# Kernel tuning notes

Measured on AMD Instinct MI355X. Metric: run time of the kernel, lower is better.

Reference implementation:

```python
import jax, jax.numpy as jnp
import numpy as np

N_NODES = 100000
N_EDGES = 1000000
D = 64
OUT = 64
EPS = 1e-5


def setup_inputs() -> dict:
    key = jax.random.key(0)
    k1, k2, k3, k4 = jax.random.split(key, 4)
    x = jax.random.normal(k1, (N_NODES, D), dtype=jnp.float32)
    edge_index = jax.random.randint(k2, (2, N_EDGES), 0, N_NODES, dtype=jnp.int64)
    # Linear(2*D, OUT): torch default init ~ U(-1/sqrt(fan_in), 1/sqrt(fan_in))
    bound = 1.0 / np.sqrt(2 * D)
    W = jax.random.uniform(k3, (2 * D, OUT), minval=-bound, maxval=bound, dtype=jnp.float32)
    b = jax.random.uniform(k4, (OUT,), minval=-bound, maxval=bound, dtype=jnp.float32)
    gamma = jnp.ones((OUT,), dtype=jnp.float32)
    beta = jnp.zeros((OUT,), dtype=jnp.float32)
    return {"x": x, "edge_index": edge_index, "W": W, "b": b, "gamma": gamma, "beta": beta}


def reference(x, edge_index, W, b, gamma, beta):
    row, col = edge_index[0], edge_index[1]
    # gather source features and scatter-add into destination nodes
    neighbor_sum = jax.ops.segment_sum(x[row], col, num_segments=x.shape[0])  # [N, D]
    h = jnp.concatenate([x, neighbor_sum], axis=-1)  # [N, 2D]
    h = h @ W + b  # [N, OUT]
    # LayerNorm over last dim
    mu = jnp.mean(h, axis=-1, keepdims=True)
    var = jnp.var(h, axis=-1, keepdims=True)
    h = (h - mu) * jax.lax.rsqrt(var + EPS) * gamma + beta
    return h
```

## Files before the change

kernel.cpp:

```cpp
#include <hip/hip_runtime.h>

#define NN 100000
#define NE 1000000
#define OUT_D 64
#define EPS 1e-5f

#define NB 196
#define COLS 512
#define BSTRIDE 6016
#define PBSTRIDE 8064
#define EPB 4096
#define NBLK1 245
#define NPROJ 1024

typedef __attribute__((ext_vector_type(8))) short bf16x8;
typedef __attribute__((ext_vector_type(4))) float f32x4;
typedef __attribute__((ext_vector_type(4))) int i32x4;

static __device__ __forceinline__ unsigned short f2bf(float f) {
    unsigned u = __float_as_uint(f);
    u += 0x7FFFu + ((u >> 16) & 1u);
    return (unsigned short)(u >> 16);
}
static __device__ __forceinline__ float bf2f(unsigned short s) {
    return __uint_as_float((unsigned)s << 16);
}

__global__ __launch_bounds__(256) void mega_kernel(
    const float* __restrict__ x, const float* __restrict__ W,
    const int* __restrict__ ei, int* __restrict__ gcur, unsigned* __restrict__ gbuf,
    unsigned short* __restrict__ y1, unsigned short* __restrict__ y2)
{
    const int tid = threadIdx.x;
    const int lane = tid & 63;
    const int wv = tid >> 6;

    if (blockIdx.x < NBLK1) {
        __shared__ int lcnt[NB];
        __shared__ int loff[NB + 1];
        __shared__ int lbase[NB];
        __shared__ int lcur[NB];
        __shared__ int wpart[4];
        __shared__ unsigned lbuf[EPB];
        __shared__ unsigned char lbkt[EPB];
        const int e0 = blockIdx.x * EPB;

        int rows[16], cols[16];
        #pragma unroll
        for (int j = 0; j < 16; ++j) {
            const int e = e0 + j * 256 + tid;
            const bool v = e < NE;
            rows[j] = v ? ei[e] : 0;
            cols[j] = v ? ei[NE + e] : -1;
        }
        for (int i = tid; i < NB; i += 256) lcnt[i] = 0;
        __syncthreads();
        #pragma unroll
        for (int j = 0; j < 16; ++j)
            if (cols[j] >= 0) atomicAdd(&lcnt[cols[j] >> 9], 1);
        __syncthreads();
        {
            const int c = (tid < NB) ? lcnt[tid] : 0;
            int s = c;
            #pragma unroll
            for (int o = 1; o < 64; o <<= 1) { int t = __shfl_up(s, o); if (lane >= o) s += t; }
            if (lane == 63) wpart[wv] = s;
            __syncthreads();
            int woff = 0;
            for (int ww = 0; ww < wv; ++ww) woff += wpart[ww];
            if (tid < NB) {
                loff[tid] = woff + s - c;
                lcur[tid] = woff + s - c;
                lbase[tid] = atomicAdd(&gcur[tid], c);
            }
            if (tid == NB - 1) loff[NB] = woff + s;
        }
        __syncthreads();
        #pragma unroll
        for (int j = 0; j < 16; ++j) {
            if (cols[j] >= 0) {
                const int b = cols[j] >> 9;
                const int p = atomicAdd(&lcur[b], 1);
                lbuf[p] = ((unsigned)rows[j] << 9) | (unsigned)(cols[j] & (COLS - 1));
                lbkt[p] = (unsigned char)b;
            }
        }
        __syncthreads();
        const int total = loff[NB];
        for (int t = tid; t < total; t += 256) {
            const int b = lbkt[t];
            const unsigned idx = (unsigned)(lbase[b] + (t - loff[b]));
            if (idx < BSTRIDE) gbuf[(size_t)b * BSTRIDE + idx] = lbuf[t];
        }
    } else {
        const int m = lane & 15;
        const int quad = lane >> 4;
        bf16x8 Wf[8][2];
        #pragma unroll
        for (int t = 0; t < 8; ++t)
            #pragma unroll
            for (int q = 0; q < 2; ++q) {
                bf16x8 f;
                #pragma unroll
                for (int j = 0; j < 8; ++j) {
                    const int k = q * 32 + quad * 8 + j;
                    const int krow = (t < 4) ? k : (64 + k);
                    const int col = (t & 3) * 16 + m;
                    f[j] = (short)f2bf(W[krow * 64 + col]);
                }
                Wf[t][q] = f;
            }
        for (int tile = (blockIdx.x - NBLK1) * 4 + wv; tile < NN / 16; tile += NPROJ * 4) {
            const int n0 = tile * 16;
            bf16x8 Af[2];
            #pragma unroll
            for (int q = 0; q < 2; ++q) {
                const float* px = x + (size_t)(n0 + m) * 64 + q * 32 + quad * 8;
                const f32x4 a0 = *(const f32x4*)px;
                const f32x4 a1 = *(const f32x4*)(px + 4);
                bf16x8 f;
                #pragma unroll
                for (int j = 0; j < 4; ++j) { f[j] = (short)f2bf(a0[j]); f[4 + j] = (short)f2bf(a1[j]); }
                Af[q] = f;
            }
            #pragma unroll
            for (int t = 0; t < 8; ++t) {
                f32x4 acc = {0.f, 0.f, 0.f, 0.f};
                acc = __builtin_amdgcn_mfma_f32_16x16x32_bf16(Af[0], Wf[t][0], acc, 0, 0, 0);
                acc = __builtin_amdgcn_mfma_f32_16x16x32_bf16(Af[1], Wf[t][1], acc, 0, 0, 0);
                unsigned short* __restrict__ dst = (t < 4) ? y1 : y2;
                const int colb = (t & 3) * 16 + m;
                #pragma unroll
                for (int r = 0; r < 4; ++r)
                    dst[(size_t)(n0 + quad * 4 + r) * 64 + colb] = f2bf(acc[r]);
            }
        }
    }
}

__global__ __launch_bounds__(256) void place_kernel(
    const int* __restrict__ gcur, const unsigned* __restrict__ gbuf,
    int* __restrict__ csr, unsigned* __restrict__ rowpack,
    unsigned short* __restrict__ y2)
{
    __shared__ int cofs[COLS + 1];
    __shared__ int ccur[COLS];
    __shared__ unsigned lsrc[BSTRIDE];
    __shared__ int ldst[PBSTRIDE];
    const int b = blockIdx.x, tid = threadIdx.x;
    const int n0 = b << 9;

    if (b == 0 && tid < 64) y2[(size_t)NN * OUT_D + tid] = 0;

    for (int i = tid; i < COLS; i += 256) cofs[i] = 0;
    for (int i = tid; i < PBSTRIDE; i += 256) ldst[i] = NN;
    __syncthreads();
    const int cntE = min(gcur[b], BSTRIDE);
    const unsigned* __restrict__ gb = gbuf + (size_t)b * BSTRIDE;

    for (int i = tid; i < cntE; i += 256) {
        const unsigned p = gb[i];
        lsrc[i] = p;
        atomicAdd(&cofs[p & (COLS - 1)], 1);
    }
    __syncthreads();
    if (tid < 64) {
        int v[8], tsum = 0;
        #pragma unroll
        for (int k = 0; k < 8; ++k) { v[k] = (cofs[tid * 8 + k] + 3) & ~3; tsum += v[k]; }
        int s = tsum;
        #pragma unroll
        for (int o = 1; o < 64; o <<= 1) { int t = __shfl_up(s, o); if (tid >= o) s += t; }
        int run = s - tsum;
        #pragma unroll
        for (int k = 0; k < 8; ++k) { cofs[tid * 8 + k] = run; ccur[tid * 8 + k] = run; run += v[k]; }
        if (tid == 63) cofs[COLS] = run;
    }
    __syncthreads();
    for (int i = tid; i < cntE; i += 256) {
        const unsigned p = lsrc[i];
        const int pos = atomicAdd(&ccur[p & (COLS - 1)], 1);
        ldst[pos] = (int)(p >> 9);
    }
    __syncthreads();
    const int ptotal = cofs[COLS];
    const int base = b * PBSTRIDE;
    for (int i = tid; i < ptotal; i += 256) csr[base + i] = ldst[i];
    const int ncols = min(COLS, NN - n0);
    for (int c = tid; c < ncols; c += 256) {
        const int st = cofs[c];
        const int len = min(cofs[c + 1] - st, 511);
        rowpack[n0 + c] = ((unsigned)st << 9) | (unsigned)len;
    }
}

__global__ __launch_bounds__(256) void out_kernel(
    const unsigned* __restrict__ rowpack, const int* __restrict__ csr,
    const unsigned short* __restrict__ y1, const unsigned short* __restrict__ y2,
    const float* __restrict__ bias, const float* __restrict__ gamma,
    const float* __restrict__ beta, float* __restrict__ out)
{
    const int lane = threadIdx.x & 63;
    const int n = __builtin_amdgcn_readfirstlane(blockIdx.x * 4 + (threadIdx.x >> 6));
    const unsigned pk = rowpack[n];
    const int cnt = (int)(pk & 511);
    const i32x4* __restrict__ cs =
        (const i32x4*)(csr + (n >> 9) * PBSTRIDE + (int)(pk >> 9));

    float acc = bf2f(y1[(size_t)n * OUT_D + lane]) + bias[lane];
    int i = 0;
    for (; i + 8 <= cnt; i += 8) {
        const i32x4 c0 = cs[(i >> 2)];
        const i32x4 c1 = cs[(i >> 2) + 1];
        const float v0 = bf2f(y2[(size_t)c0[0] * OUT_D + lane]);
        const float v1 = bf2f(y2[(size_t)c0[1] * OUT_D + lane]);
        const float v2 = bf2f(y2[(size_t)c0[2] * OUT_D + lane]);
        const float v3 = bf2f(y2[(size_t)c0[3] * OUT_D + lane]);
        const float v4 = bf2f(y2[(size_t)c1[0] * OUT_D + lane]);
        const float v5 = bf2f(y2[(size_t)c1[1] * OUT_D + lane]);
        const float v6 = bf2f(y2[(size_t)c1[2] * OUT_D + lane]);
        const float v7 = bf2f(y2[(size_t)c1[3] * OUT_D + lane]);
        acc += ((v0 + v1) + (v2 + v3)) + ((v4 + v5) + (v6 + v7));
    }
    if (i < cnt) {
        const i32x4 c0 = cs[(i >> 2)];
        const float v0 = bf2f(y2[(size_t)c0[0] * OUT_D + lane]);
        const float v1 = bf2f(y2[(size_t)c0[1] * OUT_D + lane]);
        const float v2 = bf2f(y2[(size_t)c0[2] * OUT_D + lane]);
        const float v3 = bf2f(y2[(size_t)c0[3] * OUT_D + lane]);
        acc += (v0 + v1) + (v2 + v3);
    }

    float sv = acc, sq = acc * acc;
    #pragma unroll
    for (int off = 32; off; off >>= 1) { sv += __shfl_xor(sv, off); sq += __shfl_xor(sq, off); }
    const float mu  = sv * (1.0f / OUT_D);
    const float var = sq * (1.0f / OUT_D) - mu * mu;
    const float inv = rsqrtf(var + EPS);
    out[(size_t)n * OUT_D + lane] = (acc - mu) * inv * gamma[lane] + beta[lane];
}

extern "C" void kernel_launch(void* const* d_in, const int* in_sizes, int n_in,
                              void* d_out, int out_size, void* d_ws, size_t ws_size,
                              hipStream_t stream) {
    const float* x     = (const float*)d_in[0];
    const int*   ei    = (const int*)  d_in[1];
    const float* W     = (const float*)d_in[2];
    const float* b     = (const float*)d_in[3];
    const float* gamma = (const float*)d_in[4];
    const float* beta  = (const float*)d_in[5];
    float* out = (float*)d_out;

    char* p = (char*)d_ws;
    int*            gcur    = (int*)p;             p += 1024;
    unsigned*       gbuf    = (unsigned*)p;        p += (size_t)NB * BSTRIDE * 4;
    int*            csr     = (int*)p;             p += (size_t)NB * PBSTRIDE * 4;
    unsigned*       rowpack = (unsigned*)p;        p += (size_t)(NB * COLS) * 4;
    unsigned short* y1      = (unsigned short*)p;  p += (size_t)NN * OUT_D * 2;
    unsigned short* y2      = (unsigned short*)p;

    hipMemsetAsync(gcur, 0, NB * sizeof(int), stream);
    mega_kernel <<<NBLK1 + NPROJ, 256, 0, stream>>>(x, W, ei, gcur, gbuf, y1, y2);
    place_kernel<<<NB, 256, 0, stream>>>(gcur, gbuf, csr, rowpack, y2);
    out_kernel  <<<NN / 4, 256, 0, stream>>>(rowpack, csr, y1, y2, b, gamma, beta, out);
}
```

Measured before the change: 143.4 us.

## Fuse CSR placement into aggregation kernel with per-quarter-bucket shared-memory CSR

Merges the place and out kernels into one agg_kernel. Each block handles a quarter (128 columns) of a 512-node bucket, builds that quarter's CSR in shared memory, then gathers y2 rows and applies LayerNorm directly. This removes the global csr/rowpack round trip and one kernel launch. In exchange, each bucket's edge list is read four times (once per quarter), with two passes each. Per-quarter capacity is capped at QCAP, so edges past the cap are silently dropped. The grid also shrinks to 784 blocks, each doing serial per-node work across 4 waves.

```diff
diff --git a/kernel.cpp b/kernel.cpp
--- a/kernel.cpp
+++ b/kernel.cpp
@@ -8,10 +8,12 @@
 #define NB 196
 #define COLS 512
 #define BSTRIDE 6016
-#define PBSTRIDE 8064
 #define EPB 4096
 #define NBLK1 245
 #define NPROJ 1024
+
+#define QCOLS 128
+#define QCAP 2560
 
 typedef __attribute__((ext_vector_type(8))) short bf16x8;
 typedef __attribute__((ext_vector_type(4))) float f32x4;
@@ -93,6 +95,8 @@
             if (idx < BSTRIDE) gbuf[(size_t)b * BSTRIDE + idx] = lbuf[t];
         }
     } else {
+        if (blockIdx.x == NBLK1 && tid < OUT_D)
+            y2[(size_t)NN * OUT_D + tid] = 0;
         const int m = lane & 15;
         const int quad = lane >> 4;
         bf16x8 Wf[8][2];
@@ -138,106 +142,98 @@
     }
 }
 
-__global__ __launch_bounds__(256) void place_kernel(
+__global__ __launch_bounds__(256) void agg_kernel(
     const int* __restrict__ gcur, const unsigned* __restrict__ gbuf,
-    int* __restrict__ csr, unsigned* __restrict__ rowpack,
-    unsigned short* __restrict__ y2)
-{
-    __shared__ int cofs[COLS + 1];
-    __shared__ int ccur[COLS];
-    __shared__ unsigned lsrc[BSTRIDE];
-    __shared__ int ldst[PBSTRIDE];
-    const int b = blockIdx.x, tid = threadIdx.x;
-    const int n0 = b << 9;
-
-    if (b == 0 && tid < 64) y2[(size_t)NN * OUT_D + tid] = 0;
-
-    for (int i = tid; i < COLS; i += 256) cofs[i] = 0;
-    for (int i = tid; i < PBSTRIDE; i += 256) ldst[i] = NN;
-    __syncthreads();
-    const int cntE = min(gcur[b], BSTRIDE);
-    const unsigned* __restrict__ gb = gbuf + (size_t)b * BSTRIDE;
-
-    for (int i = tid; i < cntE; i += 256) {
-        const unsigned p = gb[i];
-        lsrc[i] = p;
-        atomicAdd(&cofs[p & (COLS - 1)], 1);
-    }
-    __syncthreads();
-    if (tid < 64) {
-        int v[8], tsum = 0;
-        #pragma unroll
-        for (int k = 0; k < 8; ++k) { v[k] = (cofs[tid * 8 + k] + 3) & ~3; tsum += v[k]; }
-        int s = tsum;
-        #pragma unroll
-        for (int o = 1; o < 64; o <<= 1) { int t = __shfl_up(s, o); if (tid >= o) s += t; }
-        int run = s - tsum;
-        #pragma unroll
-        for (int k = 0; k < 8; ++k) { cofs[tid * 8 + k] = run; ccur[tid * 8 + k] = run; run += v[k]; }
-        if (tid == 63) cofs[COLS] = run;
-    }
-    __syncthreads();
-    for (int i = tid; i < cntE; i += 256) {
-        const unsigned p = lsrc[i];
-        const int pos = atomicAdd(&ccur[p & (COLS - 1)], 1);
-        ldst[pos] = (int)(p >> 9);
-    }
-    __syncthreads();
-    const int ptotal = cofs[COLS];
-    const int base = b * PBSTRIDE;
-    for (int i = tid; i < ptotal; i += 256) csr[base + i] = ldst[i];
-    const int ncols = min(COLS, NN - n0);
-    for (int c = tid; c < ncols; c += 256) {
-        const int st = cofs[c];
-        const int len = min(cofs[c + 1] - st, 511);
-        rowpack[n0 + c] = ((unsigned)st << 9) | (unsigned)len;
-    }
-}
-
-__global__ __launch_bounds__(256) void out_kernel(
-    const unsigned* __restrict__ rowpack, const int* __restrict__ csr,
     const unsigned short* __restrict__ y1, const unsigned short* __restrict__ y2,
     const float* __restrict__ bias, const float* __restrict__ gamma,
     const float* __restrict__ beta, float* __restrict__ out)
 {
-    const int lane = threadIdx.x & 63;
-    const int n = __builtin_amdgcn_readfirstlane(blockIdx.x * 4 + (threadIdx.x >> 6));
-    const unsigned pk = rowpack[n];
-    const int cnt = (int)(pk & 511);
-    const i32x4* __restrict__ cs =
-        (const i32x4*)(csr + (n >> 9) * PBSTRIDE + (int)(pk >> 9));
-
-    float acc = bf2f(y1[(size_t)n * OUT_D + lane]) + bias[lane];
-    int i = 0;
-    for (; i + 8 <= cnt; i += 8) {
-        const i32x4 c0 = cs[(i >> 2)];
-        const i32x4 c1 = cs[(i >> 2) + 1];
-        const float v0 = bf2f(y2[(size_t)c0[0] * OUT_D + lane]);
-        const float v1 = bf2f(y2[(size_t)c0[1] * OUT_D + lane]);
-        const float v2 = bf2f(y2[(size_t)c0[2] * OUT_D + lane]);
-        const float v3 = bf2f(y2[(size_t)c0[3] * OUT_D + lane]);
-        const float v4 = bf2f(y2[(size_t)c1[0] * OUT_D + lane]);
-        const float v5 = bf2f(y2[(size_t)c1[1] * OUT_D + lane]);
-        const float v6 = bf2f(y2[(size_t)c1[2] * OUT_D + lane]);
-        const float v7 = bf2f(y2[(size_t)c1[3] * OUT_D + lane]);
-        acc += ((v0 + v1) + (v2 + v3)) + ((v4 + v5) + (v6 + v7));
-    }
-    if (i < cnt) {
-        const i32x4 c0 = cs[(i >> 2)];
-        const float v0 = bf2f(y2[(size_t)c0[0] * OUT_D + lane]);
-        const float v1 = bf2f(y2[(size_t)c0[1] * OUT_D + lane]);
-        const float v2 = bf2f(y2[(size_t)c0[2] * OUT_D + lane]);
-        const float v3 = bf2f(y2[(size_t)c0[3] * OUT_D + lane]);
-        acc += (v0 + v1) + (v2 + v3);
-    }
-
-    float sv = acc, sq = acc * acc;
-    #pragma unroll
-    for (int off = 32; off; off >>= 1) { sv += __shfl_xor(sv, off); sq += __shfl_xor(sq, off); }
-    const float mu  = sv * (1.0f / OUT_D);
-    const float var = sq * (1.0f / OUT_D) - mu * mu;
-    const float inv = rsqrtf(var + EPS);
-    out[(size_t)n * OUT_D + lane] = (acc - mu) * inv * gamma[lane] + beta[lane];
+    __shared__ int cofs[QCOLS + 1];
+    __shared__ int ccur[QCOLS];
+    __shared__ int ccnt[QCOLS];
+    __shared__ int ldst[QCAP];
+    const int tid = threadIdx.x;
+    const int lane = tid & 63;
+    const int wv = tid >> 6;
+    const int b = blockIdx.x >> 2;
+    const int q = blockIdx.x & 3;
+
+    const int cntE = min(gcur[b], BSTRIDE);
+    const unsigned* __restrict__ gb = gbuf + (size_t)b * BSTRIDE;
+
+    for (int i = tid; i < QCOLS; i += 256) ccnt[i] = 0;
+    for (int i = tid; i < QCAP; i += 256) ldst[i] = NN;
+    __syncthreads();
+    for (int i = tid; i < cntE; i += 256) {
+        const unsigned p = gb[i];
+        const unsigned c9 = p & 511u;
+        if ((int)(c9 >> 7) == q) atomicAdd(&ccnt[c9 & (QCOLS - 1)], 1);
+    }
+    __syncthreads();
+    if (tid < 64) {
+        int v0 = (ccnt[2 * tid] + 3) & ~3;
+        int v1 = (ccnt[2 * tid + 1] + 3) & ~3;
+        const int tsum = v0 + v1;
+        int s = tsum;
+        #pragma unroll
+        for (int o = 1; o < 64; o <<= 1) { int t = __shfl_up(s, o); if (tid >= o) s += t; }
+        int run = s - tsum;
+        cofs[2 * tid] = run;     ccur[2 * tid] = run;     run += v0;
+        cofs[2 * tid + 1] = run; ccur[2 * tid + 1] = run; run += v1;
+        if (tid == 63) cofs[QCOLS] = run;
+    }
+    __syncthreads();
+    for (int i = tid; i < cntE; i += 256) {
+        const unsigned p = gb[i];
+        const unsigned c9 = p & 511u;
+        if ((int)(c9 >> 7) == q) {
+            const int pos = atomicAdd(&ccur[c9 & (QCOLS - 1)], 1);
+            if (pos < QCAP) ldst[pos] = (int)(p >> 9);
+        }
+    }
+    __syncthreads();
+
+    const int n0 = (b << 9) + (q << 7);
+    for (int cl = wv; cl < QCOLS; cl += 4) {
+        const int n = n0 + cl;
+        if (n >= NN) continue;
+        const int st = min(cofs[cl], QCAP);
+        const int en = min(cofs[cl + 1], QCAP);
+        const int cnt = en - st;
+        const int* __restrict__ cp = ldst + st;
+
+        float acc = bf2f(y1[(size_t)n * OUT_D + lane]) + bias[lane];
+        int i = 0;
+        for (; i + 8 <= cnt; i += 8) {
+            const i32x4 c0 = *(const i32x4*)(cp + i);
+            const i32x4 c1 = *(const i32x4*)(cp + i + 4);
+            const float v0 = bf2f(y2[(size_t)c0[0] * OUT_D + lane]);
+            const float v1 = bf2f(y2[(size_t)c0[1] * OUT_D + lane]);
+            const float v2 = bf2f(y2[(size_t)c0[2] * OUT_D + lane]);
+            const float v3 = bf2f(y2[(size_t)c0[3] * OUT_D + lane]);
+            const float v4 = bf2f(y2[(size_t)c1[0] * OUT_D + lane]);
+            const float v5 = bf2f(y2[(size_t)c1[1] * OUT_D + lane]);
+            const float v6 = bf2f(y2[(size_t)c1[2] * OUT_D + lane]);
+            const float v7 = bf2f(y2[(size_t)c1[3] * OUT_D + lane]);
+            acc += ((v0 + v1) + (v2 + v3)) + ((v4 + v5) + (v6 + v7));
+        }
+        if (i < cnt) {
+            const i32x4 c0 = *(const i32x4*)(cp + i);
+            const float v0 = bf2f(y2[(size_t)c0[0] * OUT_D + lane]);
+            const float v1 = bf2f(y2[(size_t)c0[1] * OUT_D + lane]);
+            const float v2 = bf2f(y2[(size_t)c0[2] * OUT_D + lane]);
+            const float v3 = bf2f(y2[(size_t)c0[3] * OUT_D + lane]);
+            acc += (v0 + v1) + (v2 + v3);
+        }
+
+        float sv = acc, sq = acc * acc;
+        #pragma unroll
+        for (int off = 32; off; off >>= 1) { sv += __shfl_xor(sv, off); sq += __shfl_xor(sq, off); }
+        const float mu  = sv * (1.0f / OUT_D);
+        const float var = sq * (1.0f / OUT_D) - mu * mu;
+        const float inv = rsqrtf(var + EPS);
+        out[(size_t)n * OUT_D + lane] = (acc - mu) * inv * gamma[lane] + beta[lane];
+    }
 }
 
 extern "C" void kernel_launch(void* const* d_in, const int* in_sizes, int n_in,
@@ -254,13 +250,10 @@
     char* p = (char*)d_ws;
     int*            gcur    = (int*)p;             p += 1024;
     unsigned*       gbuf    = (unsigned*)p;        p += (size_t)NB * BSTRIDE * 4;
-    int*            csr     = (int*)p;             p += (size_t)NB * PBSTRIDE * 4;
-    unsigned*       rowpack = (unsigned*)p;        p += (size_t)(NB * COLS) * 4;
     unsigned short* y1      = (unsigned short*)p;  p += (size_t)NN * OUT_D * 2;
     unsigned short* y2      = (unsigned short*)p;
 
     hipMemsetAsync(gcur, 0, NB * sizeof(int), stream);
-    mega_kernel <<<NBLK1 + NPROJ, 256, 0, stream>>>(x, W, ei, gcur, gbuf, y1, y2);
-    place_kernel<<<NB, 256, 0, stream>>>(gcur, gbuf, csr, rowpack, y2);
-    out_kernel  <<<NN / 4, 256, 0, stream>>>(rowpack, csr, y1, y2, b, gamma, beta, out);
-}
+    mega_kernel<<<NBLK1 + NPROJ, 256, 0, stream>>>(x, W, ei, gcur, gbuf, y1, y2);
+    agg_kernel <<<NB * 4,        256, 0, stream>>>(gcur, gbuf, y1, y2, b, gamma, beta, out);
+}
```

New measurement: 163.6 us. 1.14x slower.

## Stage W through LDS, widen place kernel, make out kernel persistent

Applied to the files above, without the earlier changes.

Each projection block now loads W with coalesced reads, converts it to bf16 and stores it transposed in shared memory (padded stride). It then pulls its MFMA fragments as 16-byte LDS reads, replacing the per-thread strided global gathers of W. The zeroing of the y2 padding row moves from place_kernel into the projection path. place_kernel is launched with 512 threads per block. out_kernel becomes a grid-stride loop over 2048 blocks with bias, gamma and beta hoisted out of the loop. The trade-offs are an extra LDS pass and a barrier per projection block, and fewer resident waves to hide gather latency in out_kernel.

```diff
diff --git a/kernel.cpp b/kernel.cpp
--- a/kernel.cpp
+++ b/kernel.cpp
@@ -13,6 +13,10 @@
 #define NBLK1 245
 #define NPROJ 1024
 
+#define NOUTB 2048
+
+#define WSTRIDE 136
+
 typedef __attribute__((ext_vector_type(8))) short bf16x8;
 typedef __attribute__((ext_vector_type(4))) float f32x4;
 typedef __attribute__((ext_vector_type(4))) int i32x4;
@@ -31,18 +35,19 @@
     const int* __restrict__ ei, int* __restrict__ gcur, unsigned* __restrict__ gbuf,
     unsigned short* __restrict__ y1, unsigned short* __restrict__ y2)
 {
+    __shared__ __align__(16) char smem[23648];
     const int tid = threadIdx.x;
     const int lane = tid & 63;
     const int wv = tid >> 6;
 
     if (blockIdx.x < NBLK1) {
-        __shared__ int lcnt[NB];
-        __shared__ int loff[NB + 1];
-        __shared__ int lbase[NB];
-        __shared__ int lcur[NB];
-        __shared__ int wpart[4];
-        __shared__ unsigned lbuf[EPB];
-        __shared__ unsigned char lbkt[EPB];
+        int*           lcnt  = (int*)smem;
+        int*           loff  = (int*)(smem + 784);
+        int*           lbase = (int*)(smem + 1572);
+        int*           lcur  = (int*)(smem + 2356);
+        int*           wpart = (int*)(smem + 3140);
+        unsigned*      lbuf  = (unsigned*)(smem + 3156);
+        unsigned char* lbkt  = (unsigned char*)(smem + 19540);
         const int e0 = blockIdx.x * EPB;
 
         int rows[16], cols[16];
@@ -93,6 +98,14 @@
             if (idx < BSTRIDE) gbuf[(size_t)b * BSTRIDE + idx] = lbuf[t];
         }
     } else {
+        if (blockIdx.x == NBLK1 && tid < OUT_D)
+            y2[(size_t)NN * OUT_D + tid] = 0;
+        unsigned short* wlds = (unsigned short*)smem;
+        for (int i = tid; i < 128 * 64; i += 256) {
+            const int krow = i >> 6, col = i & 63;
+            wlds[col * WSTRIDE + krow] = f2bf(W[i]);
+        }
+        __syncthreads();
         const int m = lane & 15;
         const int quad = lane >> 4;
         bf16x8 Wf[8][2];
@@ -100,15 +113,9 @@
         for (int t = 0; t < 8; ++t)
             #pragma unroll
             for (int q = 0; q < 2; ++q) {
-                bf16x8 f;
-                #pragma unroll
-                for (int j = 0; j < 8; ++j) {
-                    const int k = q * 32 + quad * 8 + j;
-                    const int krow = (t < 4) ? k : (64 + k);
-                    const int col = (t & 3) * 16 + m;
-                    f[j] = (short)f2bf(W[krow * 64 + col]);
-                }
-                Wf[t][q] = f;
+                const int krow0 = q * 32 + quad * 8 + ((t < 4) ? 0 : 64);
+                const int col = (t & 3) * 16 + m;
+                Wf[t][q] = *(const bf16x8*)(wlds + col * WSTRIDE + krow0);
             }
         for (int tile = (blockIdx.x - NBLK1) * 4 + wv; tile < NN / 16; tile += NPROJ * 4) {
             const int n0 = tile * 16;
@@ -138,10 +145,9 @@
     }
 }
 
-__global__ __launch_bounds__(256) void place_kernel(
+__global__ __launch_bounds__(512) void place_kernel(
     const int* __restrict__ gcur, const unsigned* __restrict__ gbuf,
-    int* __restrict__ csr, unsigned* __restrict__ rowpack,
-    unsigned short* __restrict__ y2)
+    int* __restrict__ csr, unsigned* __restrict__ rowpack)
 {
     __shared__ int cofs[COLS + 1];
     __shared__ int ccur[COLS];
@@ -150,15 +156,13 @@
     const int b = blockIdx.x, tid = threadIdx.x;
     const int n0 = b << 9;
 
-    if (b == 0 && tid < 64) y2[(size_t)NN * OUT_D + tid] = 0;
-
-    for (int i = tid; i < COLS; i += 256) cofs[i] = 0;
-    for (int i = tid; i < PBSTRIDE; i += 256) ldst[i] = NN;
+    for (int i = tid; i < COLS; i += 512) cofs[i] = 0;
+    for (int i = tid; i < PBSTRIDE; i += 512) ldst[i] = NN;
     __syncthreads();
     const int cntE = min(gcur[b], BSTRIDE);
     const unsigned* __restrict__ gb = gbuf + (size_t)b * BSTRIDE;
 
-    for (int i = tid; i < cntE; i += 256) {
+    for (int i = tid; i < cntE; i += 512) {
         const unsigned p = gb[i];
         lsrc[i] = p;
         atomicAdd(&cofs[p & (COLS - 1)], 1);
@@ -177,7 +181,7 @@
         if (tid == 63) cofs[COLS] = run;
     }
     __syncthreads();
-    for (int i = tid; i < cntE; i += 256) {
+    for (int i = tid; i < cntE; i += 512) {
         const unsigned p = lsrc[i];
         const int pos = atomicAdd(&ccur[p & (COLS - 1)], 1);
         ldst[pos] = (int)(p >> 9);
@@ -185,9 +189,9 @@
     __syncthreads();
     const int ptotal = cofs[COLS];
     const int base = b * PBSTRIDE;
-    for (int i = tid; i < ptotal; i += 256) csr[base + i] = ldst[i];
+    for (int i = tid; i < ptotal; i += 512) csr[base + i] = ldst[i];
     const int ncols = min(COLS, NN - n0);
-    for (int c = tid; c < ncols; c += 256) {
+    for (int c = tid; c < ncols; c += 512) {
         const int st = cofs[c];
         const int len = min(cofs[c + 1] - st, 511);
         rowpack[n0 + c] = ((unsigned)st << 9) | (unsigned)len;
@@ -201,43 +205,47 @@
     const float* __restrict__ beta, float* __restrict__ out)
 {
     const int lane = threadIdx.x & 63;
-    const int n = __builtin_amdgcn_readfirstlane(blockIdx.x * 4 + (threadIdx.x >> 6));
-    const unsigned pk = rowpack[n];
-    const int cnt = (int)(pk & 511);
-    const i32x4* __restrict__ cs =
-        (const i32x4*)(csr + (n >> 9) * PBSTRIDE + (int)(pk >> 9));
-
-    float acc = bf2f(y1[(size_t)n * OUT_D + lane]) + bias[lane];
-    int i = 0;
-    for (; i + 8 <= cnt; i += 8) {
-        const i32x4 c0 = cs[(i >> 2)];
-        const i32x4 c1 = cs[(i >> 2) + 1];
-        const float v0 = bf2f(y2[(size_t)c0[0] * OUT_D + lane]);
-        const float v1 = bf2f(y2[(size_t)c0[1] * OUT_D + lane]);
-        const float v2 = bf2f(y2[(size_t)c0[2] * OUT_D + lane]);
-        const float v3 = bf2f(y2[(size_t)c0[3] * OUT_D + lane]);
-        const float v4 = bf2f(y2[(size_t)c1[0] * OUT_D + lane]);
-        const float v5 = bf2f(y2[(size_t)c1[1] * OUT_D + lane]);
-        const float v6 = bf2f(y2[(size_t)c1[2] * OUT_D + lane]);
-        const float v7 = bf2f(y2[(size_t)c1[3] * OUT_D + lane]);
-        acc += ((v0 + v1) + (v2 + v3)) + ((v4 + v5) + (v6 + v7));
-    }
-    if (i < cnt) {
-        const i32x4 c0 = cs[(i >> 2)];
-        const float v0 = bf2f(y2[(size_t)c0[0] * OUT_D + lane]);
-        const float v1 = bf2f(y2[(size_t)c0[1] * OUT_D + lane]);
-        const float v2 = bf2f(y2[(size_t)c0[2] * OUT_D + lane]);
-        const float v3 = bf2f(y2[(size_t)c0[3] * OUT_D + lane]);
-        acc += (v0 + v1) + (v2 + v3);
-    }
-
-    float sv = acc, sq = acc * acc;
-    #pragma unroll
-    for (int off = 32; off; off >>= 1) { sv += __shfl_xor(sv, off); sq += __shfl_xor(sq, off); }
-    const float mu  = sv * (1.0f / OUT_D);
-    const float var = sq * (1.0f / OUT_D) - mu * mu;
-    const float inv = rsqrtf(var + EPS);
-    out[(size_t)n * OUT_D + lane] = (acc - mu) * inv * gamma[lane] + beta[lane];
+    const int wid0 = __builtin_amdgcn_readfirstlane(blockIdx.x * 4 + (threadIdx.x >> 6));
+    const float bi = bias[lane], ga = gamma[lane], be = beta[lane];
+
+    for (int n = wid0; n < NN; n += NOUTB * 4) {
+        const unsigned pk = rowpack[n];
+        const int cnt = (int)(pk & 511);
+        const i32x4* __restrict__ cs =
+            (const i32x4*)(csr + (n >> 9) * PBSTRIDE + (int)(pk >> 9));
+
+        float acc = bf2f(y1[(size_t)n * OUT_D + lane]) + bi;
+        int i = 0;
+        for (; i + 8 <= cnt; i += 8) {
+            const i32x4 c0 = cs[(i >> 2)];
+            const i32x4 c1 = cs[(i >> 2) + 1];
+            const float v0 = bf2f(y2[(size_t)c0[0] * OUT_D + lane]);
+            const float v1 = bf2f(y2[(size_t)c0[1] * OUT_D + lane]);
+            const float v2 = bf2f(y2[(size_t)c0[2] * OUT_D + lane]);
+            const float v3 = bf2f(y2[(size_t)c0[3] * OUT_D + lane]);
+            const float v4 = bf2f(y2[(size_t)c1[0] * OUT_D + lane]);
+            const float v5 = bf2f(y2[(size_t)c1[1] * OUT_D + lane]);
+            const float v6 = bf2f(y2[(size_t)c1[2] * OUT_D + lane]);
+            const float v7 = bf2f(y2[(size_t)c1[3] * OUT_D + lane]);
+            acc += ((v0 + v1) + (v2 + v3)) + ((v4 + v5) + (v6 + v7));
+        }
+        if (i < cnt) {
+            const i32x4 c0 = cs[(i >> 2)];
+            const float v0 = bf2f(y2[(size_t)c0[0] * OUT_D + lane]);
+            const float v1 = bf2f(y2[(size_t)c0[1] * OUT_D + lane]);
+            const float v2 = bf2f(y2[(size_t)c0[2] * OUT_D + lane]);
+            const float v3 = bf2f(y2[(size_t)c0[3] * OUT_D + lane]);
+            acc += (v0 + v1) + (v2 + v3);
+        }
+
+        float sv = acc, sq = acc * acc;
+        #pragma unroll
+        for (int off = 32; off; off >>= 1) { sv += __shfl_xor(sv, off); sq += __shfl_xor(sq, off); }
+        const float mu  = sv * (1.0f / OUT_D);
+        const float var = sq * (1.0f / OUT_D) - mu * mu;
+        const float inv = rsqrtf(var + EPS);
+        out[(size_t)n * OUT_D + lane] = (acc - mu) * inv * ga + be;
+    }
 }
 
 extern "C" void kernel_launch(void* const* d_in, const int* in_sizes, int n_in,
@@ -261,6 +269,6 @@
 
     hipMemsetAsync(gcur, 0, NB * sizeof(int), stream);
     mega_kernel <<<NBLK1 + NPROJ, 256, 0, stream>>>(x, W, ei, gcur, gbuf, y1, y2);
-    place_kernel<<<NB, 256, 0, stream>>>(gcur, gbuf, csr, rowpack, y2);
-    out_kernel  <<<NN / 4, 256, 0, stream>>>(rowpack, csr, y1, y2, b, gamma, beta, out);
-}
+    place_kernel<<<NB, 512, 0, stream>>>(gcur, gbuf, csr, rowpack);
+    out_kernel  <<<NOUTB, 256, 0, stream>>>(rowpack, csr, y1, y2, b, gamma, beta, out);
+}
```

Result: faster. 133.3 us (-7.0%).
